# Optimization experiments

Measured on AMD Instinct MI355X. Metric: run time of the kernel, lower is better.

Reference implementation:

```python
import jax, jax.numpy as jnp
import numpy as np

S = 30.0   # arcface scale
M = 0.4    # arcface angular margin
EPS = 1e-7

def setup_inputs() -> dict:
    key = jax.random.key(0)
    k1, k2, k3 = jax.random.split(key, 3)
    N, D, C = 4096, 512, 50000
    x = jax.random.normal(k1, (N, D), dtype=jnp.float32)
    # fc weight [out_fts, in_fts]; note the original's normalize loop is a no-op,
    # so W is used UN-normalized in the matmul.
    W = jax.random.normal(k2, (C, D), dtype=jnp.float32) * 0.02
    target = jax.random.randint(k3, (N,), 0, C, dtype=jnp.int32)
    return {"x": x, "W": W, "target": target}

def reference(x, W, target):
    # L2-normalize embeddings along feature dim (p=2, dim=1)
    xn = x / jnp.linalg.norm(x, axis=1, keepdims=True)
    # logits [N, C] = normalized_input @ W^T (W not normalized; see note)
    logits = jnp.einsum('nd,cd->nc', xn, W)
    # target cosine per row: diagonal(logits.T[target]) == logits[i, target[i]]
    tgt = jnp.take_along_axis(logits, target[:, None].astype(jnp.int32), axis=1)[:, 0]
    # arcface numerator: s * cos(acos(clamp(cos_t)) + m)
    numerator = S * jnp.cos(jnp.arccos(jnp.clip(tgt, -1.0 + EPS, 1.0 - EPS)) + M)
    # excl: all classes except the target column; masked exp-sum
    C = logits.shape[1]
    mask = jnp.arange(C, dtype=jnp.int32)[None, :] != target[:, None]  # [N, C]
    excl_sum = jnp.sum(jnp.where(mask, jnp.exp(S * logits), 0.0), axis=1)
    denominator = jnp.exp(numerator) + excl_sum
    L = numerator - jnp.log(denominator)
    return -jnp.mean(L)
```

## Files before the change

### kernel.cpp

```cpp
#include <hip/hip_runtime.h>
#include <hip/hip_bf16.h>

typedef __attribute__((ext_vector_type(8))) short bf16x8;
typedef __attribute__((ext_vector_type(4))) float f32x4;
typedef __attribute__((address_space(1))) const void glob_cv;
typedef __attribute__((address_space(3))) void lds_v;

constexpr int N_ = 4096, D_ = 512, C_ = 50000;
constexpr float S_ = 30.0f, M_ = 0.4f, EPS_ = 1e-7f;

#define WAITVM(N) asm volatile("s_waitcnt vmcnt(" #N ")" ::: "memory")
#define SBAR() do { __builtin_amdgcn_sched_barrier(0); __builtin_amdgcn_s_barrier(); __builtin_amdgcn_sched_barrier(0); } while (0)

__device__ inline ushort f2bf(float f) {
  unsigned u = __builtin_bit_cast(unsigned, f);
  u += 0x7fffu + ((u >> 16) & 1u);
  return (ushort)(u >> 16);
}

__global__ __launch_bounds__(256) void convw_kernel(const float* __restrict__ W,
                                                    ushort* __restrict__ Wb) {
  const long total = (long)C_ * D_ / 8;
  const long stride = (long)gridDim.x * 256;
  for (long k = (long)blockIdx.x * 256 + threadIdx.x; k < total; k += stride) {
    float4 a = reinterpret_cast<const float4*>(W)[2 * k];
    float4 b = reinterpret_cast<const float4*>(W)[2 * k + 1];
    union { ushort u[8]; uint4 v; } pk;
    pk.u[0] = f2bf(a.x); pk.u[1] = f2bf(a.y); pk.u[2] = f2bf(a.z); pk.u[3] = f2bf(a.w);
    pk.u[4] = f2bf(b.x); pk.u[5] = f2bf(b.y); pk.u[6] = f2bf(b.z); pk.u[7] = f2bf(b.w);
    reinterpret_cast<uint4*>(Wb)[k] = pk.v;
  }
}

__global__ __launch_bounds__(256) void norm_kernel(const float* __restrict__ x,
                                                   ushort* __restrict__ xnb) {
  const int wid = threadIdx.x >> 6;
  const int lane = threadIdx.x & 63;
  const int row = blockIdx.x * 4 + wid;
  const float4* xr = reinterpret_cast<const float4*>(x + (size_t)row * D_);
  float4 a = xr[lane * 2];
  float4 b = xr[lane * 2 + 1];
  float ss = a.x * a.x + a.y * a.y + a.z * a.z + a.w * a.w +
             b.x * b.x + b.y * b.y + b.z * b.z + b.w * b.w;
#pragma unroll
  for (int m = 1; m < 64; m <<= 1) ss += __shfl_xor(ss, m);
  const float inv = 1.0f / sqrtf(ss);
  union { ushort u[8]; uint4 v; } pk;
  pk.u[0] = f2bf(a.x * inv); pk.u[1] = f2bf(a.y * inv);
  pk.u[2] = f2bf(a.z * inv); pk.u[3] = f2bf(a.w * inv);
  pk.u[4] = f2bf(b.x * inv); pk.u[5] = f2bf(b.y * inv);
  pk.u[6] = f2bf(b.z * inv); pk.u[7] = f2bf(b.w * inv);
  reinterpret_cast<uint4*>(xnb + (size_t)row * D_)[lane] = pk.v;
}

__global__ __launch_bounds__(512, 2) void gemm_8ph(
    const ushort* __restrict__ A,
    const ushort* __restrict__ Wb,
    const int* __restrict__ target,
    float* __restrict__ row_sum,
    float* __restrict__ tgt_logit) {
  __shared__ char S[131072];
  __shared__ int tgt_s[256];

  const int t = threadIdx.x, lane = t & 63, wid = t >> 6;
  const int wr = wid >> 2, wc = wid & 3;

  const int orig = blockIdx.y * 16 + blockIdx.x;
  const int swz = (orig & 7) * 392 + (orig >> 3);
  const int row0 = (swz & 15) * 256, col0 = (swz >> 4) * 256;

  const int ke = ((lane & 3) ^ ((lane >> 3) & 3)) << 3;
  const int kb0 = (lane >> 4) << 4;

  auto STG = [&](int T, int kh, int isB, int buf) {
    char* dst = S + buf * 65536 + isB * 32768 + kh * 16384 + wid * 1024;
#pragma unroll
    for (int j = 0; j < 2; ++j) {
      const int r = j * 128 + wid * 16 + (lane >> 2);
      const ushort* src;
      if (isB) {
        const int gc = col0 + r;
        src = Wb + (size_t)(gc < C_ ? gc : 0) * D_ + T * 64 + kh * 32 + ke;
      } else {
        src = A + (size_t)(row0 + r) * D_ + T * 64 + kh * 32 + ke;
      }
      __builtin_amdgcn_global_load_lds((glob_cv*)src, (lds_v*)(dst + j * 8192), 16, 0, 0);
    }
  };

  f32x4 acc[8][4] = {};
  bf16x8 bf[4];

  auto PHASE = [&](int buf, int kh, int mh, auto stageFn, int wk) {
    if (mh == 0) {
      const char* Bb = S + buf * 65536 + 32768 + kh * 16384;
#pragma unroll
      for (int n = 0; n < 4; ++n) {
        const int rc = wc * 64 + n * 16 + (lane & 15);
        bf[n] = *reinterpret_cast<const bf16x8*>(Bb + rc * 64 + (kb0 ^ (((rc >> 1) & 3) << 4)));
      }
    }
    const char* Ab = S + buf * 65536 + kh * 16384;
    bf16x8 af[4];
#pragma unroll
    for (int mi = 0; mi < 4; ++mi) {
      const int rr = wr * 128 + mh * 64 + mi * 16 + (lane & 15);
      af[mi] = *reinterpret_cast<const bf16x8*>(Ab + rr * 64 + (kb0 ^ (((rr >> 1) & 3) << 4)));
    }
    stageFn();
    SBAR();
    __builtin_amdgcn_s_setprio(1);
#pragma unroll
    for (int mi = 0; mi < 4; ++mi)
#pragma unroll
      for (int n = 0; n < 4; ++n)
        acc[mh * 4 + mi][n] =
            __builtin_amdgcn_mfma_f32_16x16x32_bf16(af[mi], bf[n], acc[mh * 4 + mi][n], 0, 0, 0);
    __builtin_amdgcn_s_setprio(0);
    if (wk == 1) { WAITVM(4); }
    else if (wk == 2) { WAITVM(0); }
    SBAR();
  };

  STG(0, 0, 0, 0); STG(0, 0, 1, 0); STG(0, 1, 0, 0); STG(0, 1, 1, 0);
  STG(1, 0, 0, 1); STG(1, 0, 1, 1);
  WAITVM(4);
  SBAR();

#pragma unroll
  for (int i = 0; i < 4; ++i) {
    PHASE(0, 0, 0, [&] { STG(2 * i + 1, 1, 0, 1); }, 0);
    PHASE(0, 0, 1, [&] { STG(2 * i + 1, 1, 1, 1); }, 0);
    PHASE(0, 1, 0, [&] { if (i < 3) STG(2 * i + 2, 0, 0, 0); }, 0);
    PHASE(0, 1, 1, [&] { if (i < 3) STG(2 * i + 2, 0, 1, 0); }, i < 3 ? 1 : 2);
    PHASE(1, 0, 0, [&] { if (i < 3) STG(2 * i + 2, 1, 0, 0); }, 0);
    PHASE(1, 0, 1, [&] { if (i < 3) STG(2 * i + 2, 1, 1, 0); }, 0);
    PHASE(1, 1, 0, [&] { if (i < 3) STG(2 * i + 3, 0, 0, 1); }, 0);
    PHASE(1, 1, 1, [&] { if (i < 3) STG(2 * i + 3, 0, 1, 1); }, i < 3 ? 1 : 2);
  }

  if (t < 256) tgt_s[t] = target[row0 + t];
  __syncthreads();

#pragma unroll
  for (int mm = 0; mm < 8; ++mm) {
#pragma unroll
    for (int j = 0; j < 4; ++j) {
      const int lr = wr * 128 + mm * 16 + ((lane >> 4) << 2) + j;
      const int grow = row0 + lr;
      const int trow = tgt_s[lr];
      float s = 0.f;
#pragma unroll
      for (int n = 0; n < 4; ++n) {
        const int gcol = col0 + wc * 64 + n * 16 + (lane & 15);
        const float v = acc[mm][n][j];
        if (gcol < C_) s += __expf(S_ * v);
        if (gcol == trow) tgt_logit[grow] = v;
      }
      s += __shfl_xor(s, 1); s += __shfl_xor(s, 2);
      s += __shfl_xor(s, 4); s += __shfl_xor(s, 8);
      if ((lane & 15) == 0) atomicAdd(&row_sum[grow], s);
    }
  }
}

__global__ __launch_bounds__(256) void gemm_kernel(
    const ushort* __restrict__ A, const float* __restrict__ W,
    const int* __restrict__ target, float* __restrict__ row_sum,
    float* __restrict__ tgt_logit) {
  constexpr int BM = 128, BN = 128, BK = 64;
  __shared__ char As[BM * BK * 2];
  __shared__ char Bs[BN * BK * 2];
  __shared__ int tgt_s[BM];
  const int t = threadIdx.x;
  const int lane = t & 63, wid = t >> 6;
  const int wr = wid >> 1, wc = wid & 1;
  const int row0 = blockIdx.x * BM;
  const int col0 = blockIdx.y * BN;
  if (t < BM) tgt_s[t] = target[row0 + t];
  f32x4 acc[4][4] = {};
  for (int kt = 0; kt < D_ / BK; ++kt) {
    __syncthreads();
#pragma unroll
    for (int i = 0; i < 4; ++i) {
      const int L = i * 4096 + t * 16;
      const int r = L >> 7, kb = L & 127;
      const char* gsrc = reinterpret_cast<const char*>(A) +
                         (size_t)(row0 + r) * (D_ * 2) + kt * (BK * 2) + kb;
      uint4 v = *reinterpret_cast<const uint4*>(gsrc);
      *reinterpret_cast<uint4*>(As + r * 128 + (kb ^ ((r & 7) << 4))) = v;
    }
#pragma unroll
    for (int j = 0; j < 8; ++j) {
      const int flat = j * 256 + t;
      const int c = flat >> 4, kq = flat & 15;
      const int gc = col0 + c;
      float4 v = make_float4(0.f, 0.f, 0.f, 0.f);
      if (gc < C_)
        v = *reinterpret_cast<const float4*>(W + (size_t)gc * D_ + kt * BK + kq * 4);
      ushort4 h;
      h.x = f2bf(v.x); h.y = f2bf(v.y); h.z = f2bf(v.z); h.w = f2bf(v.w);
      const int kb = kq * 8;
      *reinterpret_cast<ushort4*>(Bs + c * 128 + (kb ^ ((c & 7) << 4))) = h;
    }
    __syncthreads();
#pragma unroll
    for (int h = 0; h < 2; ++h) {
      const int kbh = h * 64 + ((lane >> 4) << 4);
      bf16x8 af[4], bfr[4];
#pragma unroll
      for (int m = 0; m < 4; ++m) {
        const int r = wr * 64 + m * 16 + (lane & 15);
        af[m] = *reinterpret_cast<const bf16x8*>(As + r * 128 + (kbh ^ ((r & 7) << 4)));
      }
#pragma unroll
      for (int n = 0; n < 4; ++n) {
        const int c = wc * 64 + n * 16 + (lane & 15);
        bfr[n] = *reinterpret_cast<const bf16x8*>(Bs + c * 128 + (kbh ^ ((c & 7) << 4)));
      }
#pragma unroll
      for (int m = 0; m < 4; ++m)
#pragma unroll
        for (int n = 0; n < 4; ++n)
          acc[m][n] = __builtin_amdgcn_mfma_f32_16x16x32_bf16(af[m], bfr[n], acc[m][n], 0, 0, 0);
    }
  }
#pragma unroll
  for (int m = 0; m < 4; ++m) {
#pragma unroll
    for (int j = 0; j < 4; ++j) {
      const int lr = wr * 64 + m * 16 + ((lane >> 4) << 2) + j;
      const int grow = row0 + lr;
      const int trow = tgt_s[lr];
      float s = 0.f;
#pragma unroll
      for (int n = 0; n < 4; ++n) {
        const int gcol = col0 + wc * 64 + n * 16 + (lane & 15);
        const float v = acc[m][n][j];
        if (gcol < C_) s += __expf(S_ * v);
        if (gcol == trow) tgt_logit[grow] = v;
      }
      s += __shfl_xor(s, 1); s += __shfl_xor(s, 2);
      s += __shfl_xor(s, 4); s += __shfl_xor(s, 8);
      if ((lane & 15) == 0) atomicAdd(&row_sum[grow], s);
    }
  }
}

__global__ __launch_bounds__(256) void loss_kernel(const float* __restrict__ row_sum,
                                                   const float* __restrict__ tgt_logit,
                                                   float* __restrict__ out) {
  __shared__ float red[4];
  const int i = blockIdx.x * 256 + threadIdx.x;
  const float tv = tgt_logit[i];
  const float tc = fminf(fmaxf(tv, -1.0f + EPS_), 1.0f - EPS_);
  const float num = S_ * cosf(acosf(tc) + M_);
  const float excl = row_sum[i] - __expf(S_ * tv);
  const float den = __expf(num) + excl;
  float acc = num - logf(den);
#pragma unroll
  for (int m = 1; m < 64; m <<= 1) acc += __shfl_xor(acc, m);
  if ((threadIdx.x & 63) == 0) red[threadIdx.x >> 6] = acc;
  __syncthreads();
  if (threadIdx.x == 0)
    atomicAdd(out, -(red[0] + red[1] + red[2] + red[3]) / (float)N_);
}

extern "C" void kernel_launch(void* const* d_in, const int* in_sizes, int n_in,
                              void* d_out, int out_size, void* d_ws, size_t ws_size,
                              hipStream_t stream) {
  const float* x = (const float*)d_in[0];
  const float* W = (const float*)d_in[1];
  const int* target = (const int*)d_in[2];
  float* out = (float*)d_out;

  float* row_sum = (float*)d_ws;
  float* tgt_logit = row_sum + N_;
  ushort* xnb = (ushort*)(row_sum + 2 * N_);
  ushort* Wb = xnb + (size_t)N_ * D_;

  const size_t need = 2 * N_ * sizeof(float) + (size_t)N_ * D_ * 2 + (size_t)C_ * D_ * 2;

  hipMemsetAsync(d_ws, 0, 2 * N_ * sizeof(float), stream);
  hipMemsetAsync(d_out, 0, sizeof(float), stream);
  norm_kernel<<<N_ / 4, 256, 0, stream>>>(x, xnb);
  if (ws_size >= need) {
    convw_kernel<<<2048, 256, 0, stream>>>(W, Wb);
    gemm_8ph<<<dim3(16, 196), 512, 0, stream>>>(xnb, Wb, target, row_sum, tgt_logit);
  } else {
    gemm_kernel<<<dim3(N_ / 128, (C_ + 127) / 128), 256, 0, stream>>>(
        xnb, W, target, row_sum, tgt_logit);
  }
  loss_kernel<<<N_ / 256, 256, 0, stream>>>(row_sum, tgt_logit, out);
}
```

Before: 495.7 us.

## Fuse prep kernels, simplify GEMM to double-buffered K loop, single-block loss

Measured after the change: 498.1 us. No clear change (+0.5%).

```diff
diff --git a/kernel.cpp b/kernel.cpp
--- a/kernel.cpp
+++ b/kernel.cpp
@@ -18,42 +18,50 @@
   return (ushort)(u >> 16);
 }
 
-__global__ __launch_bounds__(256) void convw_kernel(const float* __restrict__ W,
-                                                    ushort* __restrict__ Wb) {
-  const long total = (long)C_ * D_ / 8;
-  const long stride = (long)gridDim.x * 256;
-  for (long k = (long)blockIdx.x * 256 + threadIdx.x; k < total; k += stride) {
-    float4 a = reinterpret_cast<const float4*>(W)[2 * k];
-    float4 b = reinterpret_cast<const float4*>(W)[2 * k + 1];
+__global__ __launch_bounds__(256) void pre_kernel(const float* __restrict__ x,
+                                                  const float* __restrict__ W,
+                                                  ushort* __restrict__ xnb,
+                                                  ushort* __restrict__ Wb,
+                                                  float* __restrict__ row_sum) {
+  const int b = blockIdx.x;
+  if (b < 2048) {
+    const long total = (long)C_ * D_ / 8;
+    const long stride = 2048L * 256;
+    for (long k = (long)b * 256 + threadIdx.x; k < total; k += stride) {
+      float4 a = reinterpret_cast<const float4*>(W)[2 * k];
+      float4 c = reinterpret_cast<const float4*>(W)[2 * k + 1];
+      union { ushort u[8]; uint4 v; } pk;
+      pk.u[0] = f2bf(a.x); pk.u[1] = f2bf(a.y); pk.u[2] = f2bf(a.z); pk.u[3] = f2bf(a.w);
+      pk.u[4] = f2bf(c.x); pk.u[5] = f2bf(c.y); pk.u[6] = f2bf(c.z); pk.u[7] = f2bf(c.w);
+      reinterpret_cast<uint4*>(Wb)[k] = pk.v;
+    }
+  } else if (b < 3072) {
+    const int wid = threadIdx.x >> 6;
+    const int lane = threadIdx.x & 63;
+    const int row = (b - 2048) * 4 + wid;
+    const float4* xr = reinterpret_cast<const float4*>(x + (size_t)row * D_);
+    float4 a = xr[lane * 2];
+    float4 c = xr[lane * 2 + 1];
+    float ss = a.x * a.x + a.y * a.y + a.z * a.z + a.w * a.w +
+               c.x * c.x + c.y * c.y + c.z * c.z + c.w * c.w;
+#pragma unroll
+    for (int m = 1; m < 64; m <<= 1) ss += __shfl_xor(ss, m);
+    const float inv = 1.0f / sqrtf(ss);
     union { ushort u[8]; uint4 v; } pk;
-    pk.u[0] = f2bf(a.x); pk.u[1] = f2bf(a.y); pk.u[2] = f2bf(a.z); pk.u[3] = f2bf(a.w);
-    pk.u[4] = f2bf(b.x); pk.u[5] = f2bf(b.y); pk.u[6] = f2bf(b.z); pk.u[7] = f2bf(b.w);
-    reinterpret_cast<uint4*>(Wb)[k] = pk.v;
-  }
-}
-
-__global__ __launch_bounds__(256) void norm_kernel(const float* __restrict__ x,
-                                                   ushort* __restrict__ xnb) {
-  const int wid = threadIdx.x >> 6;
-  const int lane = threadIdx.x & 63;
-  const int row = blockIdx.x * 4 + wid;
-  const float4* xr = reinterpret_cast<const float4*>(x + (size_t)row * D_);
-  float4 a = xr[lane * 2];
-  float4 b = xr[lane * 2 + 1];
-  float ss = a.x * a.x + a.y * a.y + a.z * a.z + a.w * a.w +
-             b.x * b.x + b.y * b.y + b.z * b.z + b.w * b.w;
-#pragma unroll
-  for (int m = 1; m < 64; m <<= 1) ss += __shfl_xor(ss, m);
-  const float inv = 1.0f / sqrtf(ss);
-  union { ushort u[8]; uint4 v; } pk;
-  pk.u[0] = f2bf(a.x * inv); pk.u[1] = f2bf(a.y * inv);
-  pk.u[2] = f2bf(a.z * inv); pk.u[3] = f2bf(a.w * inv);
-  pk.u[4] = f2bf(b.x * inv); pk.u[5] = f2bf(b.y * inv);
-  pk.u[6] = f2bf(b.z * inv); pk.u[7] = f2bf(b.w * inv);
-  reinterpret_cast<uint4*>(xnb + (size_t)row * D_)[lane] = pk.v;
-}
-
-__global__ __launch_bounds__(512, 2) void gemm_8ph(
+    pk.u[0] = f2bf(a.x * inv); pk.u[1] = f2bf(a.y * inv);
+    pk.u[2] = f2bf(a.z * inv); pk.u[3] = f2bf(a.w * inv);
+    pk.u[4] = f2bf(c.x * inv); pk.u[5] = f2bf(c.y * inv);
+    pk.u[6] = f2bf(c.z * inv); pk.u[7] = f2bf(c.w * inv);
+    reinterpret_cast<uint4*>(xnb + (size_t)row * D_)[lane] = pk.v;
+  } else {
+    float4 z = make_float4(0.f, 0.f, 0.f, 0.f);
+#pragma unroll
+    for (int i = 0; i < 8; ++i)
+      reinterpret_cast<float4*>(row_sum)[i * 256 + threadIdx.x] = z;
+  }
+}
+
+__global__ __launch_bounds__(512, 2) void gemm_m(
     const ushort* __restrict__ A,
     const ushort* __restrict__ Wb,
     const int* __restrict__ target,
@@ -89,54 +97,44 @@
   };
 
   f32x4 acc[8][4] = {};
-  bf16x8 bf[4];
-
-  auto PHASE = [&](int buf, int kh, int mh, auto stageFn, int wk) {
-    if (mh == 0) {
-      const char* Bb = S + buf * 65536 + 32768 + kh * 16384;
+
+  STG(0, 0, 0, 0); STG(0, 0, 1, 0); STG(0, 1, 0, 0); STG(0, 1, 1, 0);
+
+#pragma unroll
+  for (int kt = 0; kt < 8; ++kt) {
+    const int cur = kt & 1, nxt = cur ^ 1;
+    if (kt < 7) {
+      STG(kt + 1, 0, 0, nxt); STG(kt + 1, 0, 1, nxt);
+      STG(kt + 1, 1, 0, nxt); STG(kt + 1, 1, 1, nxt);
+    }
+    if (kt < 7) { WAITVM(8); } else { WAITVM(0); }
+    SBAR();
+
+#pragma unroll
+    for (int kh = 0; kh < 2; ++kh) {
+      const char* Ab = S + cur * 65536 + kh * 16384;
+      const char* Bb = S + cur * 65536 + 32768 + kh * 16384;
+      bf16x8 bfv[4];
 #pragma unroll
       for (int n = 0; n < 4; ++n) {
         const int rc = wc * 64 + n * 16 + (lane & 15);
-        bf[n] = *reinterpret_cast<const bf16x8*>(Bb + rc * 64 + (kb0 ^ (((rc >> 1) & 3) << 4)));
-      }
-    }
-    const char* Ab = S + buf * 65536 + kh * 16384;
-    bf16x8 af[4];
-#pragma unroll
-    for (int mi = 0; mi < 4; ++mi) {
-      const int rr = wr * 128 + mh * 64 + mi * 16 + (lane & 15);
-      af[mi] = *reinterpret_cast<const bf16x8*>(Ab + rr * 64 + (kb0 ^ (((rr >> 1) & 3) << 4)));
-    }
-    stageFn();
+        bfv[n] = *reinterpret_cast<const bf16x8*>(Bb + rc * 64 + (kb0 ^ (((rc >> 1) & 3) << 4)));
+      }
+      bf16x8 afv[8];
+#pragma unroll
+      for (int mi = 0; mi < 8; ++mi) {
+        const int rr = wr * 128 + mi * 16 + (lane & 15);
+        afv[mi] = *reinterpret_cast<const bf16x8*>(Ab + rr * 64 + (kb0 ^ (((rr >> 1) & 3) << 4)));
+      }
+      __builtin_amdgcn_s_setprio(1);
+#pragma unroll
+      for (int mi = 0; mi < 8; ++mi)
+#pragma unroll
+        for (int n = 0; n < 4; ++n)
+          acc[mi][n] = __builtin_amdgcn_mfma_f32_16x16x32_bf16(afv[mi], bfv[n], acc[mi][n], 0, 0, 0);
+      __builtin_amdgcn_s_setprio(0);
+    }
     SBAR();
-    __builtin_amdgcn_s_setprio(1);
-#pragma unroll
-    for (int mi = 0; mi < 4; ++mi)
-#pragma unroll
-      for (int n = 0; n < 4; ++n)
-        acc[mh * 4 + mi][n] =
-            __builtin_amdgcn_mfma_f32_16x16x32_bf16(af[mi], bf[n], acc[mh * 4 + mi][n], 0, 0, 0);
-    __builtin_amdgcn_s_setprio(0);
-    if (wk == 1) { WAITVM(4); }
-    else if (wk == 2) { WAITVM(0); }
-    SBAR();
-  };
-
-  STG(0, 0, 0, 0); STG(0, 0, 1, 0); STG(0, 1, 0, 0); STG(0, 1, 1, 0);
-  STG(1, 0, 0, 1); STG(1, 0, 1, 1);
-  WAITVM(4);
-  SBAR();
-
-#pragma unroll
-  for (int i = 0; i < 4; ++i) {
-    PHASE(0, 0, 0, [&] { STG(2 * i + 1, 1, 0, 1); }, 0);
-    PHASE(0, 0, 1, [&] { STG(2 * i + 1, 1, 1, 1); }, 0);
-    PHASE(0, 1, 0, [&] { if (i < 3) STG(2 * i + 2, 0, 0, 0); }, 0);
-    PHASE(0, 1, 1, [&] { if (i < 3) STG(2 * i + 2, 0, 1, 0); }, i < 3 ? 1 : 2);
-    PHASE(1, 0, 0, [&] { if (i < 3) STG(2 * i + 2, 1, 0, 0); }, 0);
-    PHASE(1, 0, 1, [&] { if (i < 3) STG(2 * i + 2, 1, 1, 0); }, 0);
-    PHASE(1, 1, 0, [&] { if (i < 3) STG(2 * i + 3, 0, 0, 1); }, 0);
-    PHASE(1, 1, 1, [&] { if (i < 3) STG(2 * i + 3, 0, 1, 1); }, i < 3 ? 1 : 2);
   }
 
   if (t < 256) tgt_s[t] = target[row0 + t];
@@ -247,23 +245,31 @@
   }
 }
 
-__global__ __launch_bounds__(256) void loss_kernel(const float* __restrict__ row_sum,
-                                                   const float* __restrict__ tgt_logit,
-                                                   float* __restrict__ out) {
-  __shared__ float red[4];
-  const int i = blockIdx.x * 256 + threadIdx.x;
-  const float tv = tgt_logit[i];
-  const float tc = fminf(fmaxf(tv, -1.0f + EPS_), 1.0f - EPS_);
-  const float num = S_ * cosf(acosf(tc) + M_);
-  const float excl = row_sum[i] - __expf(S_ * tv);
-  const float den = __expf(num) + excl;
-  float acc = num - logf(den);
+__global__ __launch_bounds__(1024) void loss_kernel(const float* __restrict__ row_sum,
+                                                    const float* __restrict__ tgt_logit,
+                                                    float* __restrict__ out) {
+  __shared__ float red[16];
+  float acc = 0.f;
+#pragma unroll
+  for (int it = 0; it < 4; ++it) {
+    const int i = it * 1024 + threadIdx.x;
+    const float tv = tgt_logit[i];
+    const float tc = fminf(fmaxf(tv, -1.0f + EPS_), 1.0f - EPS_);
+    const float num = S_ * cosf(acosf(tc) + M_);
+    const float excl = row_sum[i] - __expf(S_ * tv);
+    const float den = __expf(num) + excl;
+    acc += num - logf(den);
+  }
 #pragma unroll
   for (int m = 1; m < 64; m <<= 1) acc += __shfl_xor(acc, m);
   if ((threadIdx.x & 63) == 0) red[threadIdx.x >> 6] = acc;
   __syncthreads();
-  if (threadIdx.x == 0)
-    atomicAdd(out, -(red[0] + red[1] + red[2] + red[3]) / (float)N_);
+  if (threadIdx.x == 0) {
+    float s = 0.f;
+#pragma unroll
+    for (int w = 0; w < 16; ++w) s += red[w];
+    out[0] = -s / (float)N_;
+  }
 }
 
 extern "C" void kernel_launch(void* const* d_in, const int* in_sizes, int n_in,
@@ -281,15 +287,15 @@
 
   const size_t need = 2 * N_ * sizeof(float) + (size_t)N_ * D_ * 2 + (size_t)C_ * D_ * 2;
 
-  hipMemsetAsync(d_ws, 0, 2 * N_ * sizeof(float), stream);
-  hipMemsetAsync(d_out, 0, sizeof(float), stream);
-  norm_kernel<<<N_ / 4, 256, 0, stream>>>(x, xnb);
   if (ws_size >= need) {
-    convw_kernel<<<2048, 256, 0, stream>>>(W, Wb);
-    gemm_8ph<<<dim3(16, 196), 512, 0, stream>>>(xnb, Wb, target, row_sum, tgt_logit);
+    pre_kernel<<<3073, 256, 0, stream>>>(x, W, xnb, Wb, row_sum);
+    gemm_m<<<dim3(16, 196), 512, 0, stream>>>(xnb, Wb, target, row_sum, tgt_logit);
+    loss_kernel<<<1, 1024, 0, stream>>>(row_sum, tgt_logit, out);
   } else {
+    hipMemsetAsync(d_ws, 0, 2 * N_ * sizeof(float), stream);
+    pre_kernel<<<3073, 256, 0, stream>>>(x, W, xnb, Wb, row_sum);
     gemm_kernel<<<dim3(N_ / 128, (C_ + 127) / 128), 256, 0, stream>>>(
         xnb, W, target, row_sum, tgt_logit);
-  }
-  loss_kernel<<<N_ / 256, 256, 0, stream>>>(row_sum, tgt_logit, out);
-}
+    loss_kernel<<<1, 1024, 0, stream>>>(row_sum, tgt_logit, out);
+  }
+}
```
